# Kernel tuning notes

Measured on AMD Instinct MI355X. Metric: run time of the kernel, lower is better.

The kernel has to match this reference:

```python
import jax, jax.numpy as jnp
import numpy as np

N_NODES = 50000
N_EDGES = 800000
N_GRAPHS = 512
NUM_TYPES = 1000
EMB = 128
HID = 128


def setup_inputs() -> dict:
    key = jax.random.key(0)
    ks = jax.random.split(key, 8)
    x_type = jax.random.randint(ks[0], (N_NODES,), 0, NUM_TYPES, dtype=jnp.int32)
    edge_index = jax.random.randint(ks[1], (2, N_EDGES), 0, N_NODES, dtype=jnp.int32)
    batch = jnp.sort(jax.random.randint(ks[2], (N_NODES,), 0, N_GRAPHS, dtype=jnp.int32))
    emb = jax.random.normal(ks[3], (NUM_TYPES, EMB), jnp.float32)
    s1 = 1.0 / np.sqrt(EMB)
    s2 = 1.0 / np.sqrt(HID)
    W1 = jax.random.normal(ks[4], (EMB, HID), jnp.float32) * s1
    b1 = jnp.zeros((HID,), jnp.float32)
    W2 = jax.random.normal(ks[5], (HID, HID), jnp.float32) * s2
    b2 = jnp.zeros((HID,), jnp.float32)
    return {"x_type": x_type, "edge_index": edge_index, "batch": batch,
            "emb": emb, "W1": W1, "b1": b1, "W2": W2, "b2": b2}


def _gcn_norm(edge_index, n_nodes):
    # PyG GCNConv default: add self-loops, symmetric normalization.
    loops = jnp.arange(n_nodes, dtype=edge_index.dtype)
    src = jnp.concatenate([edge_index[0], loops])  # [E+N]
    dst = jnp.concatenate([edge_index[1], loops])
    deg = jax.ops.segment_sum(jnp.ones_like(dst, jnp.float32), dst, num_segments=n_nodes)
    dis = jax.lax.rsqrt(deg)  # deg >= 1 thanks to self-loops
    norm = dis[src] * dis[dst]  # [E+N]
    return src, dst, norm


def _gcn_conv(x, src, dst, norm, W, b, n_nodes):
    h = x @ W                                  # [N, out]
    msg = h[src] * norm[:, None]               # edge-gathered, normalized messages
    out = jax.ops.segment_sum(msg, dst, num_segments=n_nodes)  # scatter-add
    return out + b


def reference(x_type, edge_index, batch, emb, W1, b1, W2, b2):
    src, dst, norm = _gcn_norm(edge_index, N_NODES)
    x = emb[x_type]                            # [N, EMB]
    x = jax.nn.relu(_gcn_conv(x, src, dst, norm, W1, b1, N_NODES))
    x = _gcn_conv(x, src, dst, norm, W2, b2, N_NODES)
    # index_add_ pooling over graphs (dropout is identity in eval / p=0)
    out = jax.ops.segment_sum(x, batch, num_segments=N_GRAPHS)  # [G, HID]
    return out
```

## Files before the change

kernel.cpp:

```cpp
#include <hip/hip_runtime.h>

#define N_NODES 50000
#define N_EDGES 800000
#define N_GRAPHS 512
#define FDIM 128
#define NTYPES_PAD 1000

#define NBLK 128
#define CHUNK ((N_EDGES + NBLK - 1) / NBLK)
#define NQUAD (N_NODES / 4)
#define NSB ((NQUAD + 127) / 128)
#define NPW 4
#define NW ((N_NODES + NPW - 1) / NPW)

typedef __bf16 bf16x8 __attribute__((ext_vector_type(8)));
typedef float f32x4 __attribute__((ext_vector_type(4)));
union BF8 { bf16x8 v; unsigned short u[8]; };

__device__ __forceinline__ unsigned short f2bf(float f) {
  unsigned int u = __float_as_uint(f);
  unsigned int r = (u + 0x7FFFu + ((u >> 16) & 1u)) >> 16;
  return (unsigned short)r;
}
__device__ __forceinline__ float bflo(unsigned int v) {
  return __uint_as_float(v << 16);
}
__device__ __forceinline__ float bfhi(unsigned int v) {
  return __uint_as_float(v & 0xFFFF0000u);
}

__global__ __launch_bounds__(512) void k_hist(const int* __restrict__ dst,
                                              unsigned int* __restrict__ Hist,
                                              unsigned char* __restrict__ rank8,
                                              int* __restrict__ g_done) {
  __shared__ unsigned int h[NQUAD];
  int b = blockIdx.x, t = threadIdx.x;
  if (b == 0 && t == 0) *g_done = 0;
  for (int i = t; i < NQUAD; i += 512) h[i] = 0;
  __syncthreads();
  int e0 = b * CHUNK, e1 = min(e0 + CHUNK, N_EDGES);
  for (int e = e0 + t; e < e1; e += 512) {
    int d = dst[e];
    unsigned int sh = (d & 3) * 8;
    unsigned int old = atomicAdd(&h[d >> 2], 1u << sh);
    rank8[e] = (unsigned char)((old >> sh) & 0xFFu);
  }
  __syncthreads();
  unsigned int* H = Hist + (size_t)b * NQUAD;
  for (int i = t; i < NQUAD; i += 512) H[i] = h[i];
}

__global__ __launch_bounds__(128) void k_prep(
    const unsigned int* __restrict__ Hist, const int* __restrict__ batch,
    unsigned int* __restrict__ Cur, float* __restrict__ dis,
    int* __restrict__ row_ptr, float* __restrict__ Zb,
    int* __restrict__ gstart, int* __restrict__ g_bsum,
    int* __restrict__ g_done) {
  int blk = blockIdx.x, tid = threadIdx.x;
  int q = blk * 128 + tid;

  for (int i = blk * 128 + tid; i < N_GRAPHS * FDIM; i += NSB * 128)
    Zb[i] = 0.0f;

  if (q < NQUAD) {
    int i0 = 4 * q;
    int prev = (i0 == 0) ? -1 : batch[i0 - 1];
#pragma unroll
    for (int k = 0; k < 4; ++k) {
      int i = i0 + k;
      int bb = batch[i];
      for (int g = prev + 1; g <= bb; ++g) gstart[g] = i;
      prev = bb;
    }
    if (i0 + 3 == N_NODES - 1)
      for (int g = prev + 1; g <= N_GRAPHS; ++g) gstart[g] = N_NODES;
  }

  unsigned int r0 = 0, r1 = 0, r2 = 0, r3 = 0;
  if (q < NQUAD) {
    for (int b = 0; b < NBLK; ++b) {
      unsigned int v = Hist[(size_t)b * NQUAD + q];
      Cur[(size_t)b * NQUAD + q] =
          (r0 & 255u) | ((r1 & 255u) << 8) | ((r2 & 255u) << 16) | (r3 << 24);
      r0 += v & 255u;
      r1 += (v >> 8) & 255u;
      r2 += (v >> 16) & 255u;
      r3 += v >> 24;
    }
    float4 dv = make_float4(rsqrtf((float)r0 + 1.f), rsqrtf((float)r1 + 1.f),
                            rsqrtf((float)r2 + 1.f), rsqrtf((float)r3 + 1.f));
    ((float4*)dis)[q] = dv;
  }

  int tsum = (q < NQUAD) ? (int)(r0 + r1 + r2 + r3) : 0;
  __shared__ int s[128];
  s[tid] = tsum;
  __syncthreads();
  for (int d = 1; d < 128; d <<= 1) {
    int u = (tid >= d) ? s[tid - d] : 0;
    __syncthreads();
    s[tid] += u;
    __syncthreads();
  }
  int excl = s[tid] - tsum;
  int btotal = s[127];

  if (tid == 0) {
    atomicExch(&g_bsum[blk], btotal);
    __threadfence();
    atomicAdd(g_done, 1);
    while (atomicAdd(g_done, 0) < NSB) {
    }
  }
  __syncthreads();
  __shared__ int sb[NSB];
  if (tid < NSB) sb[tid] = atomicAdd(&g_bsum[tid], 0);
  __syncthreads();
  int bpref = 0;
  for (int t = 0; t < blk; ++t) bpref += sb[t];

  if (q < NQUAD) {
    int base = bpref + excl;
    ((int4*)row_ptr)[q] =
        make_int4(base, base + (int)r0, base + (int)(r0 + r1),
                  base + (int)(r0 + r1 + r2));
  }
  if (q == NQUAD - 1) row_ptr[N_NODES] = N_EDGES;
}

__global__ __launch_bounds__(512) void k_fill2(
    const int* __restrict__ src, const int* __restrict__ dst,
    const int* __restrict__ x_type, const int* __restrict__ row_ptr,
    const unsigned int* __restrict__ Cur, const unsigned char* __restrict__ rank8,
    const float* __restrict__ dis, unsigned long long* __restrict__ csr) {
  int e = blockIdx.x * blockDim.x + threadIdx.x;
  if (e >= N_EDGES) return;
  int b = e / CHUNK;
  int s = src[e], d = dst[e];
  unsigned int cw = Cur[(size_t)b * NQUAD + (d >> 2)];
  int base = (int)((cw >> ((d & 3) * 8)) & 0xFFu);
  int pos = row_ptr[d] + base + (int)rank8[e];
  unsigned int lo = (unsigned int)s | ((unsigned int)x_type[s] << 16);
  unsigned int hi = (unsigned int)f2bf(dis[d]);
  csr[pos] = (unsigned long long)lo | ((unsigned long long)hi << 32);
}

__global__ __launch_bounds__(256) void k_embw(
    const float* __restrict__ emb, const float* __restrict__ W1,
    unsigned short* __restrict__ T1) {
  __shared__ unsigned short Ws[128 * 128];
  int t = threadIdx.x, w = t >> 6, l = t & 63;
  for (int i = t; i < 16384; i += 256) {
    int k = i >> 7, n = i & 127;
    Ws[n * 128 + (k ^ ((n & 15) << 3))] = f2bf(W1[i]);
  }
  int row0 = blockIdx.x * 64 + w * 16;
  int arow = row0 + (l & 15);
  bool ok = arow < NTYPES_PAD;
  bf16x8 a[4];
#pragma unroll
  for (int ks = 0; ks < 4; ++ks) {
    BF8 av;
    const float* ap = emb + (size_t)arow * FDIM + (l >> 4) * 8 + ks * 32;
#pragma unroll
    for (int i = 0; i < 8; ++i) av.u[i] = ok ? f2bf(ap[i]) : 0;
    a[ks] = av.v;
  }
  __syncthreads();
  f32x4 acc[8] = {};
#pragma unroll
  for (int ks = 0; ks < 4; ++ks) {
#pragma unroll
    for (int ct = 0; ct < 8; ++ct) {
      int n = ct * 16 + (l & 15);
      int kk = (ks * 32 + (l >> 4) * 8) ^ ((n & 15) << 3);
      bf16x8 b = *(const bf16x8*)&Ws[n * 128 + kk];
      acc[ct] =
          __builtin_amdgcn_mfma_f32_16x16x32_bf16(a[ks], b, acc[ct], 0, 0, 0);
    }
  }
#pragma unroll
  for (int ct = 0; ct < 8; ++ct) {
    int col = ct * 16 + (l & 15);
#pragma unroll
    for (int r = 0; r < 4; ++r) {
      int row = row0 + (l >> 4) * 4 + r;
      if (row < NTYPES_PAD) T1[row * FDIM + col] = f2bf(acc[ct][r]);
    }
  }
}

__global__ void k_agg1(const int* __restrict__ x_type,
                       const unsigned short* __restrict__ T1,
                       const float* __restrict__ b1,
                       const int* __restrict__ row_ptr,
                       const unsigned long long* __restrict__ csr,
                       const float* __restrict__ dis,
                       unsigned int* __restrict__ y1) {
  int gid = blockIdx.x * blockDim.x + threadIdx.x;
  int node = gid >> 6;
  int lane = gid & 63;
  if (node >= N_NODES) return;
  const unsigned int* T = (const unsigned int*)T1;
  const unsigned int* C = (const unsigned int*)csr;
  float di = dis[node];
  unsigned int v = T[(size_t)x_type[node] * 64 + lane];
  float ax = bflo(v) * di, ay = bfhi(v) * di;
  int j = row_ptr[node], end = row_ptr[node + 1];
  for (; j + 8 <= end; j += 8) {
    unsigned int e0 = C[2 * j], e1 = C[2 * j + 2];
    unsigned int e2 = C[2 * j + 4], e3 = C[2 * j + 6];
    unsigned int e4 = C[2 * j + 8], e5 = C[2 * j + 10];
    unsigned int e6 = C[2 * j + 12], e7 = C[2 * j + 14];
    unsigned int u0 = T[(size_t)(e0 >> 16) * 64 + lane];
    unsigned int u1 = T[(size_t)(e1 >> 16) * 64 + lane];
    unsigned int u2 = T[(size_t)(e2 >> 16) * 64 + lane];
    unsigned int u3 = T[(size_t)(e3 >> 16) * 64 + lane];
    unsigned int u4 = T[(size_t)(e4 >> 16) * 64 + lane];
    unsigned int u5 = T[(size_t)(e5 >> 16) * 64 + lane];
    unsigned int u6 = T[(size_t)(e6 >> 16) * 64 + lane];
    unsigned int u7 = T[(size_t)(e7 >> 16) * 64 + lane];
    float n0 = dis[e0 & 0xFFFFu], n1 = dis[e1 & 0xFFFFu];
    float n2 = dis[e2 & 0xFFFFu], n3 = dis[e3 & 0xFFFFu];
    float n4 = dis[e4 & 0xFFFFu], n5 = dis[e5 & 0xFFFFu];
    float n6 = dis[e6 & 0xFFFFu], n7 = dis[e7 & 0xFFFFu];
    ax = fmaf(bflo(u0), n0, ax); ay = fmaf(bfhi(u0), n0, ay);
    ax = fmaf(bflo(u1), n1, ax); ay = fmaf(bfhi(u1), n1, ay);
    ax = fmaf(bflo(u2), n2, ax); ay = fmaf(bfhi(u2), n2, ay);
    ax = fmaf(bflo(u3), n3, ax); ay = fmaf(bfhi(u3), n3, ay);
    ax = fmaf(bflo(u4), n4, ax); ay = fmaf(bfhi(u4), n4, ay);
    ax = fmaf(bflo(u5), n5, ax); ay = fmaf(bfhi(u5), n5, ay);
    ax = fmaf(bflo(u6), n6, ax); ay = fmaf(bfhi(u6), n6, ay);
    ax = fmaf(bflo(u7), n7, ax); ay = fmaf(bfhi(u7), n7, ay);
  }
  for (; j + 4 <= end; j += 4) {
    unsigned int e0 = C[2 * j], e1 = C[2 * j + 2];
    unsigned int e2 = C[2 * j + 4], e3 = C[2 * j + 6];
    unsigned int u0 = T[(size_t)(e0 >> 16) * 64 + lane];
    unsigned int u1 = T[(size_t)(e1 >> 16) * 64 + lane];
    unsigned int u2 = T[(size_t)(e2 >> 16) * 64 + lane];
    unsigned int u3 = T[(size_t)(e3 >> 16) * 64 + lane];
    float n0 = dis[e0 & 0xFFFFu], n1 = dis[e1 & 0xFFFFu];
    float n2 = dis[e2 & 0xFFFFu], n3 = dis[e3 & 0xFFFFu];
    ax = fmaf(bflo(u0), n0, ax); ay = fmaf(bfhi(u0), n0, ay);
    ax = fmaf(bflo(u1), n1, ax); ay = fmaf(bfhi(u1), n1, ay);
    ax = fmaf(bflo(u2), n2, ax); ay = fmaf(bfhi(u2), n2, ay);
    ax = fmaf(bflo(u3), n3, ax); ay = fmaf(bfhi(u3), n3, ay);
  }
  for (; j < end; ++j) {
    unsigned int e = C[2 * j];
    unsigned int u = T[(size_t)(e >> 16) * 64 + lane];
    float nw = dis[e & 0xFFFFu];
    ax = fmaf(bflo(u), nw, ax);
    ay = fmaf(bfhi(u), nw, ay);
  }
  float2 bb = ((const float2*)b1)[lane];
  ax = fmaxf(fmaf(di, ax, bb.x), 0.f) * di;
  ay = fmaxf(fmaf(di, ay, bb.y), 0.f) * di;
  y1[(size_t)node * 64 + lane] = (unsigned int)f2bf(ax) |
                                 ((unsigned int)f2bf(ay) << 16);
}

__global__ void k_aggpool(const unsigned int* __restrict__ y1,
                          const int* __restrict__ row_ptr,
                          const unsigned long long* __restrict__ csr,
                          const float* __restrict__ dis,
                          const int* __restrict__ batch,
                          float* __restrict__ Partials, int* __restrict__ Gid,
                          float* __restrict__ Zb) {
  int gid = blockIdx.x * blockDim.x + threadIdx.x;
  int wid = gid >> 6;
  int lane = gid & 63;
  int n0 = wid * NPW;
  if (n0 >= N_NODES) return;
  int nend = min(n0 + NPW, N_NODES);
  int g0 = batch[n0];
  float px = 0.f, py = 0.f;
  int node = n0;
  while (node < nend) {
    int g = batch[node];
    int rend = node + 1;
    while (rend < nend && batch[rend] == g) ++rend;
    float sx = 0.f, sy = 0.f;
    for (int n = node; n < rend; ++n) {
      float dn = dis[n];
      unsigned int v = y1[(size_t)n * 64 + lane];
      sx = fmaf(dn, bflo(v), sx);
      sy = fmaf(dn, bfhi(v), sy);
    }
    int j = row_ptr[node], jend = row_ptr[rend];
    for (; j + 16 <= jend; j += 16) {
#pragma unroll
      for (int k = 0; k < 16; ++k) {
        unsigned long long e = csr[j + k];
        unsigned int u = y1[(size_t)(e & 0xFFFFu) * 64 + lane];
        float w = __uint_as_float(((unsigned int)(e >> 32)) << 16);
        sx = fmaf(bflo(u), w, sx);
        sy = fmaf(bfhi(u), w, sy);
      }
    }
    for (; j + 4 <= jend; j += 4) {
#pragma unroll
      for (int k = 0; k < 4; ++k) {
        unsigned long long e = csr[j + k];
        unsigned int u = y1[(size_t)(e & 0xFFFFu) * 64 + lane];
        float w = __uint_as_float(((unsigned int)(e >> 32)) << 16);
        sx = fmaf(bflo(u), w, sx);
        sy = fmaf(bfhi(u), w, sy);
      }
    }
    for (; j < jend; ++j) {
      unsigned long long e = csr[j];
      unsigned int u = y1[(size_t)(e & 0xFFFFu) * 64 + lane];
      float w = __uint_as_float(((unsigned int)(e >> 32)) << 16);
      sx = fmaf(bflo(u), w, sx);
      sy = fmaf(bfhi(u), w, sy);
    }
    if (g == g0) {
      px += sx;
      py += sy;
    } else {
      atomicAdd(&Zb[(size_t)g * FDIM + 2 * lane], sx);
      atomicAdd(&Zb[(size_t)g * FDIM + 2 * lane + 1], sy);
    }
    node = rend;
  }
  ((float2*)Partials)[(size_t)wid * 64 + lane] = make_float2(px, py);
  if (lane == 0) Gid[wid] = g0;
}

__global__ __launch_bounds__(128) void k_poolzw2(
    const float* __restrict__ Partials, const int* __restrict__ Gid,
    const float* __restrict__ Zb, const int* __restrict__ gstart,
    const float* __restrict__ W2, const float* __restrict__ b2,
    float* __restrict__ out) {
  __shared__ float Zs[FDIM];
  int g = blockIdx.x, t = threadIdx.x;
  int s = gstart[g], e = gstart[g + 1];
  float acc = Zb[(size_t)g * FDIM + t];
  if (e > s) {
    int w0 = s / NPW, w1 = (e - 1) / NPW;
    for (int w = w0; w <= w1; ++w)
      if (Gid[w] == g) acc += Partials[(size_t)w * FDIM + t];
  }
  Zs[t] = acc;
  __syncthreads();
  float o = 0.f;
#pragma unroll 8
  for (int k = 0; k < FDIM; ++k) o = fmaf(Zs[k], W2[k * FDIM + t], o);
  out[(size_t)g * FDIM + t] = o + (float)(e - s) * b2[t];
}

extern "C" void kernel_launch(void* const* d_in, const int* in_sizes, int n_in,
                              void* d_out, int out_size, void* d_ws,
                              size_t ws_size, hipStream_t stream) {
  const int* x_type = (const int*)d_in[0];
  const int* edge_index = (const int*)d_in[1];
  const int* batch = (const int*)d_in[2];
  const float* emb = (const float*)d_in[3];
  const float* W1 = (const float*)d_in[4];
  const float* b1 = (const float*)d_in[5];
  const float* W2 = (const float*)d_in[6];
  const float* b2 = (const float*)d_in[7];
  float* out = (float*)d_out;

  const int* src = edge_index;
  const int* dst = edge_index + N_EDGES;

  char* p = (char*)d_ws;
  size_t off = 0;
  auto alloc = [&](size_t bytes) {
    void* r = p + off;
    off = (off + bytes + 255) & ~(size_t)255;
    return r;
  };
  float* dis = (float*)alloc(N_NODES * 4);
  int* row_ptr = (int*)alloc((N_NODES + 1) * 4);
  int* gstart = (int*)alloc((N_GRAPHS + 1) * 4);
  unsigned int* Hist = (unsigned int*)alloc((size_t)NBLK * NQUAD * 4);
  unsigned int* Cur = (unsigned int*)alloc((size_t)NBLK * NQUAD * 4);
  unsigned char* rank8 = (unsigned char*)alloc(N_EDGES);
  unsigned long long* csr =
      (unsigned long long*)alloc((size_t)N_EDGES * 8);
  unsigned short* T1 = (unsigned short*)alloc((size_t)NTYPES_PAD * FDIM * 2);
  unsigned int* y1 = (unsigned int*)alloc((size_t)N_NODES * 64 * 4);
  float* Partials = (float*)alloc((size_t)NW * FDIM * 4);
  int* Gid = (int*)alloc(NW * 4);
  float* Zb = (float*)alloc((size_t)N_GRAPHS * FDIM * 4);
  int* g_bsum = (int*)alloc(NSB * 4);
  int* g_done = (int*)alloc(4);
  (void)ws_size;

  k_hist<<<NBLK, 512, 0, stream>>>(dst, Hist, rank8, g_done);
  k_prep<<<NSB, 128, 0, stream>>>(Hist, batch, Cur, dis, row_ptr, Zb, gstart,
                                  g_bsum, g_done);
  k_fill2<<<(N_EDGES + 511) / 512, 512, 0, stream>>>(
      src, dst, x_type, row_ptr, Cur, rank8, dis, csr);
  k_embw<<<(NTYPES_PAD + 63) / 64, 256, 0, stream>>>(emb, W1, T1);
  k_agg1<<<(N_NODES * 64 + 255) / 256, 256, 0, stream>>>(
      x_type, T1, b1, row_ptr, csr, dis, y1);
  k_aggpool<<<(NW * 64 + 255) / 256, 256, 0, stream>>>(
      y1, row_ptr, csr, dis, batch, Partials, Gid, Zb);
  k_poolzw2<<<N_GRAPHS, 128, 0, stream>>>(Partials, Gid, Zb, gstart, W2, b2,
                                          out);
}
```

Before: 151.3 us.

## Fuse embedding-W1 GEMM into prep kernel and retune prep and pooling granularity

Moves the emb@W1 MFMA table computation into extra blocks of the prep kernel, so it runs alongside the degree scan and one launch disappears. The prep scan block grows from 128 to 256 threads, halving the number of spinning blocks in the grid-wide barrier, and shared memory is reused for both roles. Nodes per wave in the pooled aggregation drops from 4 to 2, which adds more waves and more partial rows. The prep kernel now reserves 32KB of shared memory per block, and it depends on all scan blocks being co-resident for the spin barrier.

```diff
diff --git a/kernel.cpp b/kernel.cpp
--- a/kernel.cpp
+++ b/kernel.cpp
@@ -9,8 +9,9 @@
 #define NBLK 128
 #define CHUNK ((N_EDGES + NBLK - 1) / NBLK)
 #define NQUAD (N_NODES / 4)
-#define NSB ((NQUAD + 127) / 128)
-#define NPW 4
+#define NSB ((NQUAD + 255) / 256)
+#define EMBW_BLOCKS 16
+#define NPW 2
 #define NW ((N_NODES + NPW - 1) / NPW)
 
 typedef __bf16 bf16x8 __attribute__((ext_vector_type(8)));
@@ -50,16 +51,64 @@
   for (int i = t; i < NQUAD; i += 512) H[i] = h[i];
 }
 
-__global__ __launch_bounds__(128) void k_prep(
+__global__ __launch_bounds__(256) void k_prep(
     const unsigned int* __restrict__ Hist, const int* __restrict__ batch,
     unsigned int* __restrict__ Cur, float* __restrict__ dis,
     int* __restrict__ row_ptr, float* __restrict__ Zb,
     int* __restrict__ gstart, int* __restrict__ g_bsum,
-    int* __restrict__ g_done) {
+    int* __restrict__ g_done, const float* __restrict__ emb,
+    const float* __restrict__ W1, unsigned short* __restrict__ T1) {
+  __shared__ unsigned short sh[16384];
   int blk = blockIdx.x, tid = threadIdx.x;
-  int q = blk * 128 + tid;
-
-  for (int i = blk * 128 + tid; i < N_GRAPHS * FDIM; i += NSB * 128)
+
+  if (blk >= NSB) {
+    unsigned short* Ws = sh;
+    int t = tid, w = t >> 6, l = t & 63;
+    for (int i = t; i < 16384; i += 256) {
+      int k = i >> 7, n = i & 127;
+      Ws[n * 128 + (k ^ ((n & 15) << 3))] = f2bf(W1[i]);
+    }
+    int row0 = (blk - NSB) * 64 + w * 16;
+    int arow = row0 + (l & 15);
+    bool ok = arow < NTYPES_PAD;
+    bf16x8 a[4];
+#pragma unroll
+    for (int ks = 0; ks < 4; ++ks) {
+      BF8 av;
+      const float* ap = emb + (size_t)arow * FDIM + (l >> 4) * 8 + ks * 32;
+#pragma unroll
+      for (int i = 0; i < 8; ++i) av.u[i] = ok ? f2bf(ap[i]) : 0;
+      a[ks] = av.v;
+    }
+    __syncthreads();
+    f32x4 acc[8] = {};
+#pragma unroll
+    for (int ks = 0; ks < 4; ++ks) {
+#pragma unroll
+      for (int ct = 0; ct < 8; ++ct) {
+        int n = ct * 16 + (l & 15);
+        int kk = (ks * 32 + (l >> 4) * 8) ^ ((n & 15) << 3);
+        bf16x8 b = *(const bf16x8*)&Ws[n * 128 + kk];
+        acc[ct] =
+            __builtin_amdgcn_mfma_f32_16x16x32_bf16(a[ks], b, acc[ct], 0, 0, 0);
+      }
+    }
+#pragma unroll
+    for (int ct = 0; ct < 8; ++ct) {
+      int col = ct * 16 + (l & 15);
+#pragma unroll
+      for (int r = 0; r < 4; ++r) {
+        int row = row0 + (l >> 4) * 4 + r;
+        if (row < NTYPES_PAD) T1[row * FDIM + col] = f2bf(acc[ct][r]);
+      }
+    }
+    return;
+  }
+
+  int* si = (int*)sh;
+  int q = blk * 256 + tid;
+
+  for (int i = blk * 256 + tid; i < N_GRAPHS * FDIM; i += NSB * 256)
     Zb[i] = 0.0f;
 
   if (q < NQUAD) {
@@ -93,17 +142,16 @@
   }
 
   int tsum = (q < NQUAD) ? (int)(r0 + r1 + r2 + r3) : 0;
-  __shared__ int s[128];
-  s[tid] = tsum;
-  __syncthreads();
-  for (int d = 1; d < 128; d <<= 1) {
-    int u = (tid >= d) ? s[tid - d] : 0;
+  si[tid] = tsum;
+  __syncthreads();
+  for (int d = 1; d < 256; d <<= 1) {
+    int u = (tid >= d) ? si[tid - d] : 0;
     __syncthreads();
-    s[tid] += u;
+    si[tid] += u;
     __syncthreads();
   }
-  int excl = s[tid] - tsum;
-  int btotal = s[127];
+  int excl = si[tid] - tsum;
+  int btotal = si[255];
 
   if (tid == 0) {
     atomicExch(&g_bsum[blk], btotal);
@@ -113,7 +161,7 @@
     }
   }
   __syncthreads();
-  __shared__ int sb[NSB];
+  int* sb = si + 256;
   if (tid < NSB) sb[tid] = atomicAdd(&g_bsum[tid], 0);
   __syncthreads();
   int bpref = 0;
@@ -143,51 +191,6 @@
   unsigned int lo = (unsigned int)s | ((unsigned int)x_type[s] << 16);
   unsigned int hi = (unsigned int)f2bf(dis[d]);
   csr[pos] = (unsigned long long)lo | ((unsigned long long)hi << 32);
-}
-
-__global__ __launch_bounds__(256) void k_embw(
-    const float* __restrict__ emb, const float* __restrict__ W1,
-    unsigned short* __restrict__ T1) {
-  __shared__ unsigned short Ws[128 * 128];
-  int t = threadIdx.x, w = t >> 6, l = t & 63;
-  for (int i = t; i < 16384; i += 256) {
-    int k = i >> 7, n = i & 127;
-    Ws[n * 128 + (k ^ ((n & 15) << 3))] = f2bf(W1[i]);
-  }
-  int row0 = blockIdx.x * 64 + w * 16;
-  int arow = row0 + (l & 15);
-  bool ok = arow < NTYPES_PAD;
-  bf16x8 a[4];
-#pragma unroll
-  for (int ks = 0; ks < 4; ++ks) {
-    BF8 av;
-    const float* ap = emb + (size_t)arow * FDIM + (l >> 4) * 8 + ks * 32;
-#pragma unroll
-    for (int i = 0; i < 8; ++i) av.u[i] = ok ? f2bf(ap[i]) : 0;
-    a[ks] = av.v;
-  }
-  __syncthreads();
-  f32x4 acc[8] = {};
-#pragma unroll
-  for (int ks = 0; ks < 4; ++ks) {
-#pragma unroll
-    for (int ct = 0; ct < 8; ++ct) {
-      int n = ct * 16 + (l & 15);
-      int kk = (ks * 32 + (l >> 4) * 8) ^ ((n & 15) << 3);
-      bf16x8 b = *(const bf16x8*)&Ws[n * 128 + kk];
-      acc[ct] =
-          __builtin_amdgcn_mfma_f32_16x16x32_bf16(a[ks], b, acc[ct], 0, 0, 0);
-    }
-  }
-#pragma unroll
-  for (int ct = 0; ct < 8; ++ct) {
-    int col = ct * 16 + (l & 15);
-#pragma unroll
-    for (int r = 0; r < 4; ++r) {
-      int row = row0 + (l >> 4) * 4 + r;
-      if (row < NTYPES_PAD) T1[row * FDIM + col] = f2bf(acc[ct][r]);
-    }
-  }
 }
 
 __global__ void k_agg1(const int* __restrict__ x_type,
@@ -392,11 +395,10 @@
   (void)ws_size;
 
   k_hist<<<NBLK, 512, 0, stream>>>(dst, Hist, rank8, g_done);
-  k_prep<<<NSB, 128, 0, stream>>>(Hist, batch, Cur, dis, row_ptr, Zb, gstart,
-                                  g_bsum, g_done);
+  k_prep<<<NSB + EMBW_BLOCKS, 256, 0, stream>>>(
+      Hist, batch, Cur, dis, row_ptr, Zb, gstart, g_bsum, g_done, emb, W1, T1);
   k_fill2<<<(N_EDGES + 511) / 512, 512, 0, stream>>>(
       src, dst, x_type, row_ptr, Cur, rank8, dis, csr);
-  k_embw<<<(NTYPES_PAD + 63) / 64, 256, 0, stream>>>(emb, W1, T1);
   k_agg1<<<(N_NODES * 64 + 255) / 256, 256, 0, stream>>>(
       x_type, T1, b1, row_ptr, csr, dis, y1);
   k_aggpool<<<(NW * 64 + 255) / 256, 256, 0, stream>>>(
```

New measurement: 148.3 us. -2.0%, faster.
